# Kernel optimization log

Hardware: AMD Instinct MI355X
Metric: run time of the kernel (lower is better)

Reference implementation:

```python
import jax, jax.numpy as jnp
import numpy as np

C = 256
HEADS = 4
HIDDEN = 4 * C  # LeFF default hidden_dim = dim*4
EPS = 1e-5


def conv2d(x, w, pad):
    # x: [B,C,H,W], w: [O,I,kh,kw]
    return jax.lax.conv_general_dilated(
        x, w, window_strides=(1, 1), padding=[(pad, pad), (pad, pad)],
        dimension_numbers=('NCHW', 'OIHW', 'NCHW'))


def dwconv2d(x, w, pad):
    # depthwise: w: [C,1,kh,kw], groups = C
    return jax.lax.conv_general_dilated(
        x, w, window_strides=(1, 1), padding=[(pad, pad), (pad, pad)],
        dimension_numbers=('NCHW', 'OIHW', 'NCHW'),
        feature_group_count=x.shape[1])


def conv1x1(x, w):
    # w: [O, I]; pointwise conv as einsum
    return jnp.einsum('oi,bihw->bohw', w, x)


def layernorm(x, weight, bias):
    # WithBias LayerNorm over channel dim of NCHW (matches to_3d -> LN over c)
    mu = jnp.mean(x, axis=1, keepdims=True)
    var = jnp.mean((x - mu) ** 2, axis=1, keepdims=True)
    xn = (x - mu) / jnp.sqrt(var + EPS)
    return xn * weight[None, :, None, None] + bias[None, :, None, None]


def mhsa(q, k, v, heads):
    # q,k,v: [B,C,H,W] -> global attention over N = H*W tokens
    b, c, h, w = q.shape
    d = c // heads
    scale = d ** -0.5
    def split(t):
        return t.reshape(b, heads, d, h * w)  # [B,H,d,N]
    qh, kh, vh = split(q), split(k), split(v)
    attn = jnp.einsum('bhdn,bhdm->bhnm', qh, kh) * scale  # [B,H,N,N]
    attn = jax.nn.softmax(attn, axis=-1)
    out = jnp.einsum('bhnm,bhdm->bhdn', attn, vh)
    return out.reshape(b, c, h, w)


def self_attn(x, w_qkv, w_proj, heads):
    qkv = conv1x1(x, w_qkv)  # [B,3C,H,W]
    q, k, v = jnp.split(qkv, 3, axis=1)
    return conv1x1(mhsa(q, k, v, heads), w_proj)


def cross_attn(qf, kvf, w_q, w_k, w_v, w_proj, heads):
    q = conv1x1(qf, w_q)
    k = conv1x1(kvf, w_k)
    v = conv1x1(kvf, w_v)
    return conv1x1(mhsa(q, k, v, heads), w_proj)


def leff(x, w_in, w_dw, w_out):
    h = conv1x1(x, w_in)
    h = dwconv2d(h, w_dw, pad=1)
    h = jax.nn.gelu(h, approximate=False)  # torch nn.GELU() = exact erf
    return conv1x1(h, w_out)


def setup_inputs() -> dict:
    key = jax.random.key(0)
    ks = jax.random.split(key, 32)
    s = 0.02
    inp = {
        'aop_feat': jax.random.normal(ks[0], (8, C, 32, 32), jnp.float32),
        'dop_feat': jax.random.normal(ks[1], (8, C, 32, 32), jnp.float32),
        'w_qconv': jax.random.normal(ks[2], (C, C, 3, 3), jnp.float32) * s,
        'w_kvconv': jax.random.normal(ks[3], (C, C, 5, 5), jnp.float32) * s,
        'lnq1_w': jnp.ones((C,), jnp.float32), 'lnq1_b': jnp.zeros((C,), jnp.float32),
        'lnkv1_w': jnp.ones((C,), jnp.float32), 'lnkv1_b': jnp.zeros((C,), jnp.float32),
        'lnq2_w': jnp.ones((C,), jnp.float32), 'lnq2_b': jnp.zeros((C,), jnp.float32),
        'lnkv2_w': jnp.ones((C,), jnp.float32), 'lnkv2_b': jnp.zeros((C,), jnp.float32),
        'lnffn_w': jnp.ones((C,), jnp.float32), 'lnffn_b': jnp.zeros((C,), jnp.float32),
        'saq_qkv': jax.random.normal(ks[4], (3 * C, C), jnp.float32) * s,
        'saq_proj': jax.random.normal(ks[5], (C, C), jnp.float32) * s,
        'sakv_qkv': jax.random.normal(ks[6], (3 * C, C), jnp.float32) * s,
        'sakv_proj': jax.random.normal(ks[7], (C, C), jnp.float32) * s,
        'ca_q': jax.random.normal(ks[8], (C, C), jnp.float32) * s,
        'ca_k': jax.random.normal(ks[9], (C, C), jnp.float32) * s,
        'ca_v': jax.random.normal(ks[10], (C, C), jnp.float32) * s,
        'ca_proj': jax.random.normal(ks[11], (C, C), jnp.float32) * s,
        'leff_in': jax.random.normal(ks[12], (HIDDEN, C), jnp.float32) * s,
        'leff_dw': jax.random.normal(ks[13], (HIDDEN, 1, 3, 3), jnp.float32) * s,
        'leff_out': jax.random.normal(ks[14], (C, HIDDEN), jnp.float32) * s,
    }
    return inp


def reference(aop_feat, dop_feat, w_qconv, w_kvconv,
              lnq1_w, lnq1_b, lnkv1_w, lnkv1_b, lnq2_w, lnq2_b,
              lnkv2_w, lnkv2_b, lnffn_w, lnffn_b,
              saq_qkv, saq_proj, sakv_qkv, sakv_proj,
              ca_q, ca_k, ca_v, ca_proj,
              leff_in, leff_dw, leff_out):
    # q branch
    q_branch = conv2d(aop_feat, w_qconv, pad=1)
    q_branch = q_branch + self_attn(layernorm(q_branch, lnq1_w, lnq1_b), saq_qkv, saq_proj, HEADS)
    q = layernorm(q_branch, lnq2_w, lnq2_b)
    # kv branch
    kv_branch = conv2d(dop_feat, w_kvconv, pad=2)
    kv_branch = kv_branch + self_attn(layernorm(kv_branch, lnkv1_w, lnkv1_b), sakv_qkv, sakv_proj, HEADS)
    kv = layernorm(kv_branch, lnkv2_w, lnkv2_b)
    # cross attention + FFN
    x = q_branch + cross_attn(q, kv, ca_q, ca_k, ca_v, ca_proj, HEADS)
    x = x + leff(layernorm(x, lnffn_w, lnffn_b), leff_in, leff_dw, leff_out)
    return x
```

## Files before the change

### kernel.cpp

```cpp
#include <hip/hip_runtime.h>
#include <hip/hip_bf16.h>


using bf16 = __hip_bfloat16;
typedef short v8s __attribute__((ext_vector_type(8)));
typedef float v4f  __attribute__((ext_vector_type(4)));

static __device__ __forceinline__ float bf2f(bf16 x) { return __bfloat162float(x); }
static __device__ __forceinline__ float us2f(unsigned short u)
{ union { unsigned int i; float f; } x; x.i = ((unsigned)u) << 16; return x.f; }
static __device__ __forceinline__ unsigned short f2us(float f)
{ bf16 h = __float2bfloat16(f); return *(unsigned short*)&h; }
static __device__ __forceinline__ float ldi(const void* p, size_t i, int isbf)
{ return isbf ? bf2f(((const bf16*)p)[i]) : ((const float*)p)[i]; }

__global__ void detect_kernel(const unsigned short* p, int* flag)
{
    if (threadIdx.x == 0 && blockIdx.x == 0)
        *flag = (p[0] == 0x3F80) ? 1 : 0;
}

struct CvtArgs { const void* src[20]; unsigned off[21]; };

__global__ __launch_bounds__(256) void pre_all(
    CvtArgs a,
    const void* __restrict__ s0, const void* __restrict__ s1,
    const void* __restrict__ W3, const void* __restrict__ W5,
    const void* __restrict__ Wdw, const int* __restrict__ flag,
    bf16* __restrict__ canon,
    bf16* __restrict__ d0, bf16* __restrict__ d1,
    bf16* __restrict__ R3, bf16* __restrict__ R5, bf16* __restrict__ Rdw)
{
    __shared__ float T[64][65];
    int bx = blockIdx.x, t = threadIdx.x;
    int isbf = *flag;
    if (bx < 5130) {
        unsigned e = bx * 256u + t;
        int s = 0;
        while (e >= a.off[s + 1]) ++s;
        canon[e] = __float2bfloat16(ldi(a.src[s], e - a.off[s], isbf));
    } else if (bx < 6154) {
        int i = bx - 5130;
        int x = i & 15, y = (i >> 4) & 3, z = i >> 6;
        const void* src = (z < 8) ? s0 : s1;
        bf16* dst       = (z < 8) ? d0 : d1;
        int hw0 = x * 64, c0 = y * 64, b = z & 7;
        int c = t >> 2, x16 = (t & 3) * 16;
        size_t sbase = ((size_t)b * 256 + c0 + c) * 1024 + hw0 + x16;
#pragma unroll
        for (int j = 0; j < 16; ++j) T[c][x16 + j] = ldi(src, sbase + j, isbf);
        __syncthreads();
        int hw = t >> 2, c16 = (t & 3) * 16;
        bf16* dp = dst + ((size_t)(b << 10) + hw0 + hw) * 256 + c0 + c16;
#pragma unroll
        for (int j = 0; j < 16; ++j) dp[j] = __float2bfloat16(T[c16 + j][hw]);
    } else {
        int idx = (bx - 6154) * 256 + t;
        if (idx < 589824) {
            int ci = idx & 255, o = (idx >> 8) & 255, khkw = idx >> 16;
            int kh = khkw / 3, kw = khkw % 3;
            R3[idx] = __float2bfloat16(
                ldi(W3, (((size_t)o * 256 + ci) * 3 + kh) * 3 + kw, isbf));
        } else if (idx < 2228224) {
            int j = idx - 589824;
            int ci = j & 255, o = (j >> 8) & 255, khkw = j >> 16;
            int kh = khkw / 5, kw = khkw % 5;
            R5[j] = __float2bfloat16(
                ldi(W5, (((size_t)o * 256 + ci) * 5 + kh) * 5 + kw, isbf));
        } else {
            int j = idx - 2228224;
            int c = j & 1023, tap = j >> 10;
            Rdw[j] = __float2bfloat16(ldi(Wdw, (size_t)c * 9 + tap, isbf));
        }
    }
}

static __device__ __forceinline__ void gemm_store(
    bf16* __restrict__ Yb, float* __restrict__ Yf, bf16* __restrict__ Y2,
    const bf16* __restrict__ R, int mode, int Ochan,
    int mm, int nn, float v)
{
    if (mode == 0) {
        size_t off = (size_t)mm * Ochan + nn;
        if (R) v += bf2f(R[off]);
        Yb[off] = __float2bfloat16(v);
    } else if (mode == 1) {
        Yb[((size_t)(nn >> 10) * Ochan + mm) * 1024 + (nn & 1023)] =
            __float2bfloat16(v);
    } else if (mode == 2) {
        Yf[((size_t)(nn >> 10) * Ochan + mm) * 1024 + (nn & 1023)] =
            v + bf2f(R[(size_t)nn * 256 + mm]);
    } else if (mode == 3) {
        if (mm < 512) Yb[(size_t)nn * 512 + mm] = __float2bfloat16(v);
        else Y2[((size_t)(nn >> 10) * 256 + (mm - 512)) * 1024 + (nn & 1023)] =
                 __float2bfloat16(v);
    } else {
        Yb[(size_t)nn * 512 + Ochan + mm] = __float2bfloat16(v);
    }
}

static __device__ __forceinline__ void mgemm_core(
    const short* __restrict__ MA, const short* __restrict__ MB,
    bf16* __restrict__ Yb, float* __restrict__ Yf, bf16* __restrict__ Y2,
    const bf16* __restrict__ R, int K, int mode, int Ochan,
    short As[64][72], short Bs[64][72])
{
    int m0 = blockIdx.x * 64, n0 = blockIdx.y * 64;
    int t = threadIdx.x, lane = t & 63, wv = t >> 6;
    int l15 = lane & 15, quad = lane >> 4;
    int srow = t >> 2, scol = (t & 3) * 16;

    const short* pa = &MA[(size_t)(m0 + srow) * K + scol];
    const short* pb = &MB[(size_t)(n0 + srow) * K + scol];

    v4f acc[4] = {};
    v8s ra0 = *(const v8s*)&pa[0], ra1 = *(const v8s*)&pa[8];
    v8s rb0 = *(const v8s*)&pb[0], rb1 = *(const v8s*)&pb[8];

    for (int k0 = 0; k0 < K; k0 += 64) {
        if (k0) __syncthreads();
        *(v8s*)&As[srow][scol]     = ra0;
        *(v8s*)&As[srow][scol + 8] = ra1;
        *(v8s*)&Bs[srow][scol]     = rb0;
        *(v8s*)&Bs[srow][scol + 8] = rb1;
        __syncthreads();
        if (k0 + 64 < K) {
            ra0 = *(const v8s*)&pa[k0 + 64];
            ra1 = *(const v8s*)&pa[k0 + 72];
            rb0 = *(const v8s*)&pb[k0 + 64];
            rb1 = *(const v8s*)&pb[k0 + 72];
        }
#pragma unroll
        for (int kk = 0; kk < 2; ++kk) {
            v8s a = *(const v8s*)&As[wv * 16 + l15][kk * 32 + quad * 8];
#pragma unroll
            for (int nt = 0; nt < 4; ++nt) {
                v8s b = *(const v8s*)&Bs[nt * 16 + l15][kk * 32 + quad * 8];
                acc[nt] = __builtin_amdgcn_mfma_f32_16x16x32_bf16(a, b, acc[nt], 0, 0, 0);
            }
        }
    }

#pragma unroll
    for (int nt = 0; nt < 4; ++nt)
#pragma unroll
        for (int r = 0; r < 4; ++r)
            gemm_store(Yb, Yf, Y2, R, mode, Ochan,
                       m0 + wv * 16 + quad * 4 + r,
                       n0 + nt * 16 + l15, acc[nt][r]);
}

__global__ __launch_bounds__(256) void mgemm(
    const short* __restrict__ MA, const short* __restrict__ MB,
    bf16* __restrict__ Yb, float* __restrict__ Yf, bf16* __restrict__ Y2,
    const bf16* __restrict__ R, int K, int mode, int Ochan)
{
    __shared__ short As[64][72], Bs[64][72];
    mgemm_core(MA, MB, Yb, Yf, Y2, R, K, mode, Ochan, As, Bs);
}

struct GA { const short* A; const short* B; bf16* Yb; float* Yf; bf16* Y2;
            const bf16* R; int K; int mode; int Oc; };
struct GA3 { GA g[3]; };

__global__ __launch_bounds__(256) void mgemm_z(GA3 P)
{
    __shared__ short As[64][72], Bs[64][72];
    const GA& a = P.g[blockIdx.z];
    mgemm_core(a.A, a.B, a.Yb, a.Yf, a.Y2, a.R, a.K, a.mode, a.Oc, As, Bs);
}

template <int KS, int PAD>
static __device__ __forceinline__ void mconv128_core(
    const short* __restrict__ Xn, const short* __restrict__ Wr,
    bf16* __restrict__ Y, float* __restrict__ Yf,
    short As[128][72], short Bs[128][72],
    int p0, int o0, int kbeg, int kend)
{
    int t = threadIdx.x, lane = t & 63, wv = t >> 6;
    int l15 = lane & 15, quad = lane >> 4;
    int wm = wv >> 1, wn = wv & 1;
    int srow = t >> 1, scol = (t & 1) * 32;

    int p  = p0 + srow;
    int hw = p & 1023, hh = hw >> 5, ww = hw & 31;
    size_t ib = ((size_t)(p >> 10)) << 10;

    v4f acc[4][4] = {};
    v8s ra[4], rb[4];

    auto ldk = [&](int k0) {
        int khkw = k0 >> 8;
        int kh = khkw / KS, kw = khkw % KS;
        int hi = hh + kh - PAD, wi = ww + kw - PAD;
        int aci = (k0 & 255) + scol;
        v8s z = {0, 0, 0, 0, 0, 0, 0, 0};
        ra[0] = z; ra[1] = z; ra[2] = z; ra[3] = z;
        if ((unsigned)hi < 32u && (unsigned)wi < 32u) {
            const short* sa = &Xn[(ib + (hi << 5) + wi) * 256 + aci];
            ra[0] = *(const v8s*)&sa[0];  ra[1] = *(const v8s*)&sa[8];
            ra[2] = *(const v8s*)&sa[16]; ra[3] = *(const v8s*)&sa[24];
        }
        const short* sb = &Wr[((size_t)khkw * 256 + o0 + srow) * 256 + (k0 & 255) + scol];
        rb[0] = *(const v8s*)&sb[0];  rb[1] = *(const v8s*)&sb[8];
        rb[2] = *(const v8s*)&sb[16]; rb[3] = *(const v8s*)&sb[24];
    };

    ldk(kbeg);

    for (int k0 = kbeg; k0 < kend; k0 += 64) {
        if (k0 != kbeg) __syncthreads();
        *(v8s*)&As[srow][scol]      = ra[0];
        *(v8s*)&As[srow][scol + 8]  = ra[1];
        *(v8s*)&As[srow][scol + 16] = ra[2];
        *(v8s*)&As[srow][scol + 24] = ra[3];
        *(v8s*)&Bs[srow][scol]      = rb[0];
        *(v8s*)&Bs[srow][scol + 8]  = rb[1];
        *(v8s*)&Bs[srow][scol + 16] = rb[2];
        *(v8s*)&Bs[srow][scol + 24] = rb[3];
        __syncthreads();
        if (k0 + 64 < kend) ldk(k0 + 64);
#pragma unroll
        for (int kk = 0; kk < 2; ++kk) {
            v8s af[4], bf[4];
#pragma unroll
            for (int i = 0; i < 4; ++i)
                af[i] = *(const v8s*)&As[wm * 64 + i * 16 + l15][kk * 32 + quad * 8];
#pragma unroll
            for (int i = 0; i < 4; ++i)
                bf[i] = *(const v8s*)&Bs[wn * 64 + i * 16 + l15][kk * 32 + quad * 8];
#pragma unroll
            for (int mt = 0; mt < 4; ++mt)
#pragma unroll
                for (int nt = 0; nt < 4; ++nt)
                    acc[mt][nt] = __builtin_amdgcn_mfma_f32_16x16x32_bf16(
                        af[mt], bf[nt], acc[mt][nt], 0, 0, 0);
        }
    }

#pragma unroll
    for (int mt = 0; mt < 4; ++mt)
#pragma unroll
        for (int nt = 0; nt < 4; ++nt)
#pragma unroll
            for (int r = 0; r < 4; ++r) {
                int pp = p0 + wm * 64 + mt * 16 + quad * 4 + r;
                int oo = o0 + wn * 64 + nt * 16 + l15;
                if (Yf) Yf[(size_t)pp * 256 + oo] = acc[mt][nt][r];
                else    Y[(size_t)pp * 256 + oo] = __float2bfloat16(acc[mt][nt][r]);
            }
}

__global__ __launch_bounds__(256) void mconv2(
    const short* __restrict__ Xa, const short* __restrict__ Wa, bf16* __restrict__ Ya,
    const short* __restrict__ Xb, const short* __restrict__ Wb,
    float* __restrict__ P0, float* __restrict__ P1, float* __restrict__ P2)
{
    __shared__ short As[128][72];
    __shared__ short Bs[128][72];
    int wg = blockIdx.x;
    if (wg < 128) {
        mconv128_core<3, 1>(Xa, Wa, Ya, nullptr, As, Bs,
                            (wg & 63) * 128, (wg >> 6) * 128, 0, 2304);
    } else {
        int j = wg - 128;
        int part = j >> 7, xy = j & 127;
        float* Pf = (part == 0) ? P0 : (part == 1) ? P1 : P2;
        int kbeg = part * 2112;
        int kend = (part < 2) ? kbeg + 2112 : 6400;
        mconv128_core<5, 2>(Xb, Wb, nullptr, Pf, As, Bs,
                            (xy & 63) * 128, (xy >> 6) * 128, kbeg, kend);
    }
}

__global__ __launch_bounds__(256) void addcvt3(
    const float* __restrict__ A, const float* __restrict__ B,
    const float* __restrict__ C, bf16* __restrict__ Y)
{
    int i = (blockIdx.x * 256 + threadIdx.x) * 4;
    float4 a = *(const float4*)&A[i];
    float4 b = *(const float4*)&B[i];
    float4 c = *(const float4*)&C[i];
    ushort4 o;
    o.x = f2us(a.x + b.x + c.x);
    o.y = f2us(a.y + b.y + c.y);
    o.z = f2us(a.z + b.z + c.z);
    o.w = f2us(a.w + b.w + c.w);
    *(ushort4*)((unsigned short*)Y + i) = o;
}

static __device__ __forceinline__ void attn_core(
    const bf16* __restrict__ QK, const bf16* __restrict__ V,
    bf16* __restrict__ Out, int b, int h, int n0,
    short Ps[4][16][72], short Ks[64][72], short Vs[64][72])
{
    int t = threadIdx.x, lane = t & 63, wv = t >> 6;
    int l15 = lane & 15, quad = lane >> 4;
    int srow = t >> 2, scol = (t & 3) * 16;

    const short* qk = (const short*)QK;
    const short* vp = (const short*)V + ((size_t)b * 256 + h * 64) * 1024;

    size_t qrow = ((size_t)b * 1024 + n0 + wv * 16 + l15) * 512 + h * 64;
    v8s qf0 = *(const v8s*)&qk[qrow + quad * 8];
    v8s qf1 = *(const v8s*)&qk[qrow + 32 + quad * 8];

    v4f oacc[4] = {};
    float mi[4], li[4], nmiSC[4];
#pragma unroll
    for (int r = 0; r < 4; ++r) { mi[r] = -1e30f; li[r] = 0.f; nmiSC[r] = 0.f; }
    const float SC = 0.18033688011112042f;

    const short* kbase = &qk[((size_t)b * 1024 + srow) * 512 + 256 + h * 64 + scol];
    const short* vbase = vp + (size_t)srow * 1024 + scol;

    v8s rk0 = *(const v8s*)&kbase[0], rk1 = *(const v8s*)&kbase[8];
    v8s rv0 = *(const v8s*)&vbase[0], rv1 = *(const v8s*)&vbase[8];

    for (int m0 = 0; m0 < 1024; m0 += 64) {
        if (m0) __syncthreads();
        *(v8s*)&Ks[srow][scol]     = rk0;
        *(v8s*)&Ks[srow][scol + 8] = rk1;
        *(v8s*)&Vs[srow][scol]     = rv0;
        *(v8s*)&Vs[srow][scol + 8] = rv1;
        __syncthreads();
        if (m0 + 64 < 1024) {
            rk0 = *(const v8s*)&kbase[(size_t)(m0 + 64) * 512];
            rk1 = *(const v8s*)&kbase[(size_t)(m0 + 64) * 512 + 8];
            rv0 = *(const v8s*)&vbase[m0 + 64];
            rv1 = *(const v8s*)&vbase[m0 + 72];
        }

        v4f sacc[4];
        __builtin_amdgcn_s_setprio(1);
#pragma unroll
        for (int ct = 0; ct < 4; ++ct) {
            v8s kf0 = *(const v8s*)&Ks[ct * 16 + l15][quad * 8];
            v8s kf1 = *(const v8s*)&Ks[ct * 16 + l15][32 + quad * 8];
            v4f z = {0.f, 0.f, 0.f, 0.f};
            z = __builtin_amdgcn_mfma_f32_16x16x32_bf16(qf0, kf0, z, 0, 0, 0);
            z = __builtin_amdgcn_mfma_f32_16x16x32_bf16(qf1, kf1, z, 0, 0, 0);
            sacc[ct] = z;
        }
        __builtin_amdgcn_s_setprio(0);

        float pr[4];
#pragma unroll
        for (int r = 0; r < 4; ++r)
            pr[r] = fmaxf(fmaxf(sacc[0][r], sacc[1][r]),
                          fmaxf(sacc[2][r], sacc[3][r]));
        bool grow = (pr[0] > mi[0]) | (pr[1] > mi[1]) |
                    (pr[2] > mi[2]) | (pr[3] > mi[3]);
        if (__any(grow)) {
#pragma unroll
            for (int mk = 1; mk <= 8; mk <<= 1)
#pragma unroll
                for (int r = 0; r < 4; ++r)
                    pr[r] = fmaxf(pr[r], __shfl_xor(pr[r], mk));
#pragma unroll
            for (int r = 0; r < 4; ++r) {
                float mn = fmaxf(mi[r], pr[r]);
                float al = exp2f((mi[r] - mn) * SC);
                mi[r] = mn;
                nmiSC[r] = -mn * SC;
                li[r] *= al;
#pragma unroll
                for (int dt = 0; dt < 4; ++dt) oacc[dt][r] *= al;
            }
        }

#pragma unroll
        for (int ct = 0; ct < 4; ++ct)
#pragma unroll
            for (int r = 0; r < 4; ++r) {
                float pvv = exp2f(fmaf(sacc[ct][r], SC, nmiSC[r]));
                li[r] += pvv;
                Ps[wv][quad * 4 + r][ct * 16 + l15] = (short)f2us(pvv);
            }

        v8s pf0 = *(const v8s*)&Ps[wv][l15][quad * 8];
        v8s pf1 = *(const v8s*)&Ps[wv][l15][32 + quad * 8];
        __builtin_amdgcn_s_setprio(1);
#pragma unroll
        for (int dt = 0; dt < 4; ++dt) {
            v8s vf0 = *(const v8s*)&Vs[dt * 16 + l15][quad * 8];
            v8s vf1 = *(const v8s*)&Vs[dt * 16 + l15][32 + quad * 8];
            oacc[dt] = __builtin_amdgcn_mfma_f32_16x16x32_bf16(pf0, vf0, oacc[dt], 0, 0, 0);
            oacc[dt] = __builtin_amdgcn_mfma_f32_16x16x32_bf16(pf1, vf1, oacc[dt], 0, 0, 0);
        }
        __builtin_amdgcn_s_setprio(0);
    }

#pragma unroll
    for (int mk = 1; mk <= 8; mk <<= 1)
#pragma unroll
        for (int r = 0; r < 4; ++r)
            li[r] += __shfl_xor(li[r], mk);

    float linv[4];
#pragma unroll
    for (int r = 0; r < 4; ++r) linv[r] = 1.0f / li[r];
    size_t pb = (size_t)b * 1024 + n0 + wv * 16;
#pragma unroll
    for (int dt = 0; dt < 4; ++dt)
#pragma unroll
        for (int r = 0; r < 4; ++r)
            Out[(pb + quad * 4 + r) * 256 + h * 64 + dt * 16 + l15] =
                __float2bfloat16(oacc[dt][r] * linv[r]);
}

template <int NG>
__global__ __launch_bounds__(256) void attn_swz(
    const bf16* __restrict__ QK0, const bf16* __restrict__ V0, bf16* __restrict__ O0,
    const bf16* __restrict__ QK1, const bf16* __restrict__ V1, bf16* __restrict__ O1)
{
    __shared__ short Ps[4][16][72];
    __shared__ short Ks[64][72], Vs[64][72];
    int i = blockIdx.x;
    int xcd = i & 7, idx = i >> 3;
    int g = xcd * (NG / 8) + (idx >> 4);
    int n0 = (idx & 15) * 64;
    int h = g & 3, zz = g >> 2;
    int b = zz & 7;
    if (zz < 8) attn_core(QK0, V0, O0, b, h, n0, Ps, Ks, Vs);
    else        attn_core(QK1, V1, O1, b, h, n0, Ps, Ks, Vs);
}

static __device__ __forceinline__ void ln_row(
    const bf16* __restrict__ X, const bf16* __restrict__ g,
    const bf16* __restrict__ be, bf16* __restrict__ Y, size_t p)
{
    int lane = threadIdx.x & 63;
    const ushort4 u = *(const ushort4*)(X + p * 256 + lane * 4);
    float v0 = us2f(u.x), v1 = us2f(u.y), v2 = us2f(u.z), v3 = us2f(u.w);
    float s = v0 + v1 + v2 + v3;
    float ss = v0 * v0 + v1 * v1 + v2 * v2 + v3 * v3;
#pragma unroll
    for (int off = 32; off; off >>= 1) {
        s  += __shfl_xor(s, off);
        ss += __shfl_xor(ss, off);
    }
    float mu   = s * (1.0f / 256.0f);
    float var  = ss * (1.0f / 256.0f) - mu * mu;
    float rstd = rsqrtf(fmaxf(var, 0.0f) + 1e-5f);
    const ushort4 gu = *(const ushort4*)((const unsigned short*)g + lane * 4);
    const ushort4 bu = *(const ushort4*)((const unsigned short*)be + lane * 4);
    ushort4 o;
    o.x = f2us((v0 - mu) * rstd * us2f(gu.x) + us2f(bu.x));
    o.y = f2us((v1 - mu) * rstd * us2f(gu.y) + us2f(bu.y));
    o.z = f2us((v2 - mu) * rstd * us2f(gu.z) + us2f(bu.z));
    o.w = f2us((v3 - mu) * rstd * us2f(gu.w) + us2f(bu.w));
    *(ushort4*)(Y + p * 256 + lane * 4) = o;
}

__global__ __launch_bounds__(256) void ln_nhwc(
    const bf16* __restrict__ X, const bf16* __restrict__ g,
    const bf16* __restrict__ be, bf16* __restrict__ Y)
{
    int wv = threadIdx.x >> 6;
    ln_row(X, g, be, Y, (size_t)blockIdx.x * 4 + wv);
}

__global__ __launch_bounds__(256) void ln_nhwc2(
    const bf16* __restrict__ X0, const bf16* __restrict__ g0,
    const bf16* __restrict__ b0, bf16* __restrict__ Y0,
    const bf16* __restrict__ X1, const bf16* __restrict__ g1,
    const bf16* __restrict__ b1, bf16* __restrict__ Y1)
{
    int wv = threadIdx.x >> 6;
    int sel = blockIdx.x >> 11;
    size_t p = (size_t)(blockIdx.x & 2047) * 4 + wv;
    if (sel == 0) ln_row(X0, g0, b0, Y0, p);
    else          ln_row(X1, g1, b1, Y1, p);
}

__global__ __launch_bounds__(256) void dwgelu_nhwc(
    const bf16* __restrict__ H, const bf16* __restrict__ Wr,
    bf16* __restrict__ Y)
{
    int idx = blockIdx.x * 256 + threadIdx.x;
    int p = idx >> 7, c8 = (idx & 127) * 8;
    int hw = p & 1023, hh = hw >> 5, ww = hw & 31;
    size_t ib = ((size_t)(p >> 10)) << 10;
    float acc[8] = {};
#pragma unroll
    for (int kh = 0; kh < 3; ++kh)
#pragma unroll
        for (int kw = 0; kw < 3; ++kw) {
            int hi = hh + kh - 1, wi = ww + kw - 1;
            if ((unsigned)hi < 32u && (unsigned)wi < 32u) {
                v8s hv = *(const v8s*)((const short*)H + (ib + (hi << 5) + wi) * 1024 + c8);
                v8s wvv = *(const v8s*)((const short*)Wr + (kh * 3 + kw) * 1024 + c8);
#pragma unroll
                for (int j = 0; j < 8; ++j)
                    acc[j] = fmaf(us2f((unsigned short)wvv[j]),
                                  us2f((unsigned short)hv[j]), acc[j]);
            }
        }
    short ov[8];
#pragma unroll
    for (int j = 0; j < 8; ++j) {
        float x = acc[j];
        ov[j] = (short)f2us(0.5f * x * (1.0f + erff(x * 0.70710678118654752f)));
    }
    v8s o = {ov[0], ov[1], ov[2], ov[3], ov[4], ov[5], ov[6], ov[7]};
    *(v8s*)((short*)Y + (size_t)p * 1024 + c8) = o;
}

extern "C" void kernel_launch(void* const* d_in, const int* in_sizes, int n_in,
                              void* d_out, int out_size, void* d_ws, size_t ws_size,
                              hipStream_t stream)
{
    static const int  lidx[20] = {4,5,6,7,8,9,10,11,12,13,14,15,16,17,18,19,20,21,22,24};
    static const unsigned lsz[20] = {256,256,256,256,256,256,256,256,256,256,
                                     196608,65536,196608,65536,
                                     65536,65536,65536,65536,262144,262144};
    CvtArgs args;
    unsigned pre[21]; pre[0] = 0;
    for (int i = 0; i < 20; ++i) {
        args.src[i] = d_in[lidx[i]];
        pre[i + 1] = pre[i] + lsz[i];
    }
    for (int i = 0; i < 21; ++i) args.off[i] = pre[i];
    const unsigned ltot = pre[20];

    int*  flag  = (int*)d_ws;
    bf16* canon = (bf16*)d_ws + 128;
    bf16* cn[25];
    for (int i = 0; i < 20; ++i) cn[lidx[i]] = canon + pre[i];

    bf16* Wr3  = canon + ltot;
    bf16* Wr5  = Wr3 + 589824;
    bf16* Wdwr = Wr5 + 1638400;
    const size_t SZ = 2097152;
    bf16* slab = Wdwr + 9216;
    bf16* qb   = slab + 0 * SZ;
    bf16* kvb  = slab + 1 * SZ;
    bf16* t0   = slab + 2 * SZ;
    bf16* q    = slab + 3 * SZ;
    bf16* kv   = slab + 4 * SZ;
    bf16* QKb  = slab + 5 * SZ;
    bf16* Vb   = slab + 7 * SZ;
    bf16* t1   = slab + 8 * SZ;
    bf16* QK2  = slab + 9 * SZ;
    bf16* V2   = slab + 11 * SZ;
    bf16* aopT = slab + 9 * SZ;
    bf16* dopT = slab + 10 * SZ;
    bf16* hb   = slab + 3 * SZ;
    bf16* h2   = slab + 7 * SZ;
    float* P0f = (float*)(slab + 2 * SZ);
    float* P1f = (float*)(slab + 4 * SZ);
    float* P2f = (float*)(slab + 6 * SZ);
    float* out = (float*)d_out;

    dim3 blk(256);
    auto S = [](const bf16* p) { return (const short*)p; };

    detect_kernel<<<1, 64, 0, stream>>>((const unsigned short*)d_in[4], flag);
    pre_all<<<5130 + 1024 + 8740, blk, 0, stream>>>(
        args, d_in[0], d_in[1], d_in[2], d_in[3], d_in[23], flag,
        canon, aopT, dopT, Wr3, Wr5, Wdwr);

    mconv2<<<512, blk, 0, stream>>>(S(aopT), (const short*)Wr3, qb,
                                    S(dopT), (const short*)Wr5, P0f, P1f, P2f);
    addcvt3<<<2048, blk, 0, stream>>>(P0f, P1f, P2f, kvb);

    ln_nhwc2<<<4096, blk, 0, stream>>>(qb, cn[4], cn[5], t0,
                                       kvb, cn[6], cn[7], t1);
    GA3 P;
    P.g[0] = GA{S(cn[14]), S(t0), QKb, nullptr, Vb, nullptr, 256, 3, 0};
    P.g[1] = GA{S(cn[16]), S(t1), QK2, nullptr, V2, nullptr, 256, 3, 0};
    P.g[2] = P.g[1];
    mgemm_z<<<dim3(12, 128, 2), blk, 0, stream>>>(P);

    attn_swz<64><<<1024, blk, 0, stream>>>(QKb, Vb, t0, QK2, V2, t1);

    P.g[0] = GA{S(t0), S(cn[15]), qb, nullptr, nullptr, qb, 256, 0, 256};
    P.g[1] = GA{S(t1), S(cn[17]), kvb, nullptr, nullptr, kvb, 256, 0, 256};
    P.g[2] = P.g[1];
    mgemm_z<<<dim3(128, 4, 2), blk, 0, stream>>>(P);

    ln_nhwc2<<<4096, blk, 0, stream>>>(qb, cn[8], cn[9], q,
                                       kvb, cn[10], cn[11], kv);

    P.g[0] = GA{S(cn[18]), S(q),  QKb, nullptr, nullptr, nullptr, 256, 4, 0};
    P.g[1] = GA{S(cn[19]), S(kv), QKb, nullptr, nullptr, nullptr, 256, 4, 256};
    P.g[2] = GA{S(cn[20]), S(kv), Vb,  nullptr, nullptr, nullptr, 256, 1, 256};
    mgemm_z<<<dim3(4, 128, 3), blk, 0, stream>>>(P);

    attn_swz<32><<<512, blk, 0, stream>>>(QKb, Vb, t0, QKb, Vb, t0);
    mgemm<<<dim3(128, 4), blk, 0, stream>>>(S(t0), S(cn[21]), qb, nullptr, nullptr, qb, 256, 0, 256);

    ln_nhwc<<<2048, blk, 0, stream>>>(qb, cn[12], cn[13], t0);
    mgemm<<<dim3(128, 16), blk, 0, stream>>>(S(t0), S(cn[22]), hb, nullptr, nullptr, nullptr, 256, 0, 1024);
    dwgelu_nhwc<<<4096, blk, 0, stream>>>(hb, Wdwr, h2);
    mgemm<<<dim3(4, 128), blk, 0, stream>>>(S(cn[24]), S(h2), nullptr, out, nullptr, qb, 1024, 2, 256);
}
```

Baseline: 402.2 us.

## Keep attention probabilities in registers via transposed MFMA and permuted K rows

The QK^T and PV MFMAs now have their operands swapped, so each lane holds scores for a single query row. K rows are read with a permutation chosen so that the exp'd probabilities can be packed directly into the B operand of the PV MFMA. This removes the Ps shared-memory round trip and cuts the row-max and row-sum shuffles from four per row to two. Output stores become vectorized 4-element writes. The cost is subtle index bookkeeping that must be exactly right for correctness.

```diff
diff --git a/kernel.cpp b/kernel.cpp
--- a/kernel.cpp
+++ b/kernel.cpp
@@ -292,7 +292,7 @@
 static __device__ __forceinline__ void attn_core(
     const bf16* __restrict__ QK, const bf16* __restrict__ V,
     bf16* __restrict__ Out, int b, int h, int n0,
-    short Ps[4][16][72], short Ks[64][72], short Vs[64][72])
+    short Ks[64][72], short Vs[64][72])
 {
     int t = threadIdx.x, lane = t & 63, wv = t >> 6;
     int l15 = lane & 15, quad = lane >> 4;
@@ -306,10 +306,13 @@
     v8s qf1 = *(const v8s*)&qk[qrow + 32 + quad * 8];
 
     v4f oacc[4] = {};
-    float mi[4], li[4], nmiSC[4];
-#pragma unroll
-    for (int r = 0; r < 4; ++r) { mi[r] = -1e30f; li[r] = 0.f; nmiSC[r] = 0.f; }
+    float mi = -1e30f, li = 0.f, nmi = 0.f;
     const float SC = 0.18033688011112042f;
+
+    int sig[4];
+#pragma unroll
+    for (int ct = 0; ct < 4; ++ct)
+        sig[ct] = ((ct & 1) << 5) + ((l15 >> 2) << 3) + ((ct >> 1) << 2) + (l15 & 3);
 
     const short* kbase = &qk[((size_t)b * 1024 + srow) * 512 + 256 + h * 64 + scol];
     const short* vbase = vp + (size_t)srow * 1024 + scol;
@@ -335,78 +338,74 @@
         __builtin_amdgcn_s_setprio(1);
 #pragma unroll
         for (int ct = 0; ct < 4; ++ct) {
-            v8s kf0 = *(const v8s*)&Ks[ct * 16 + l15][quad * 8];
-            v8s kf1 = *(const v8s*)&Ks[ct * 16 + l15][32 + quad * 8];
+            v8s kf0 = *(const v8s*)&Ks[sig[ct]][quad * 8];
+            v8s kf1 = *(const v8s*)&Ks[sig[ct]][32 + quad * 8];
             v4f z = {0.f, 0.f, 0.f, 0.f};
-            z = __builtin_amdgcn_mfma_f32_16x16x32_bf16(qf0, kf0, z, 0, 0, 0);
-            z = __builtin_amdgcn_mfma_f32_16x16x32_bf16(qf1, kf1, z, 0, 0, 0);
+            z = __builtin_amdgcn_mfma_f32_16x16x32_bf16(kf0, qf0, z, 0, 0, 0);
+            z = __builtin_amdgcn_mfma_f32_16x16x32_bf16(kf1, qf1, z, 0, 0, 0);
             sacc[ct] = z;
         }
         __builtin_amdgcn_s_setprio(0);
 
-        float pr[4];
-#pragma unroll
-        for (int r = 0; r < 4; ++r)
-            pr[r] = fmaxf(fmaxf(sacc[0][r], sacc[1][r]),
-                          fmaxf(sacc[2][r], sacc[3][r]));
-        bool grow = (pr[0] > mi[0]) | (pr[1] > mi[1]) |
-                    (pr[2] > mi[2]) | (pr[3] > mi[3]);
-        if (__any(grow)) {
-#pragma unroll
-            for (int mk = 1; mk <= 8; mk <<= 1)
-#pragma unroll
-                for (int r = 0; r < 4; ++r)
-                    pr[r] = fmaxf(pr[r], __shfl_xor(pr[r], mk));
+        float pm = sacc[0][0];
+#pragma unroll
+        for (int ct = 0; ct < 4; ++ct)
+#pragma unroll
+            for (int r = 0; r < 4; ++r) pm = fmaxf(pm, sacc[ct][r]);
+        if (__any(pm > mi)) {
+            pm = fmaxf(pm, __shfl_xor(pm, 16));
+            pm = fmaxf(pm, __shfl_xor(pm, 32));
+            float mn = fmaxf(mi, pm);
+            float al = exp2f((mi - mn) * SC);
+            mi = mn;
+            nmi = -mn * SC;
+            li *= al;
+#pragma unroll
+            for (int dt = 0; dt < 4; ++dt)
+#pragma unroll
+                for (int r = 0; r < 4; ++r) oacc[dt][r] *= al;
+        }
+
+        short pv[4][4];
+#pragma unroll
+        for (int ct = 0; ct < 4; ++ct)
 #pragma unroll
             for (int r = 0; r < 4; ++r) {
-                float mn = fmaxf(mi[r], pr[r]);
-                float al = exp2f((mi[r] - mn) * SC);
-                mi[r] = mn;
-                nmiSC[r] = -mn * SC;
-                li[r] *= al;
-#pragma unroll
-                for (int dt = 0; dt < 4; ++dt) oacc[dt][r] *= al;
+                float pvv = exp2f(fmaf(sacc[ct][r], SC, nmi));
+                li += pvv;
+                pv[ct][r] = (short)f2us(pvv);
             }
-        }
-
-#pragma unroll
-        for (int ct = 0; ct < 4; ++ct)
-#pragma unroll
-            for (int r = 0; r < 4; ++r) {
-                float pvv = exp2f(fmaf(sacc[ct][r], SC, nmiSC[r]));
-                li[r] += pvv;
-                Ps[wv][quad * 4 + r][ct * 16 + l15] = (short)f2us(pvv);
-            }
-
-        v8s pf0 = *(const v8s*)&Ps[wv][l15][quad * 8];
-        v8s pf1 = *(const v8s*)&Ps[wv][l15][32 + quad * 8];
+
+        v8s pf0 = {pv[0][0], pv[0][1], pv[0][2], pv[0][3],
+                   pv[2][0], pv[2][1], pv[2][2], pv[2][3]};
+        v8s pf1 = {pv[1][0], pv[1][1], pv[1][2], pv[1][3],
+                   pv[3][0], pv[3][1], pv[3][2], pv[3][3]};
+
         __builtin_amdgcn_s_setprio(1);
 #pragma unroll
         for (int dt = 0; dt < 4; ++dt) {
             v8s vf0 = *(const v8s*)&Vs[dt * 16 + l15][quad * 8];
             v8s vf1 = *(const v8s*)&Vs[dt * 16 + l15][32 + quad * 8];
-            oacc[dt] = __builtin_amdgcn_mfma_f32_16x16x32_bf16(pf0, vf0, oacc[dt], 0, 0, 0);
-            oacc[dt] = __builtin_amdgcn_mfma_f32_16x16x32_bf16(pf1, vf1, oacc[dt], 0, 0, 0);
+            oacc[dt] = __builtin_amdgcn_mfma_f32_16x16x32_bf16(vf0, pf0, oacc[dt], 0, 0, 0);
+            oacc[dt] = __builtin_amdgcn_mfma_f32_16x16x32_bf16(vf1, pf1, oacc[dt], 0, 0, 0);
         }
         __builtin_amdgcn_s_setprio(0);
     }
 
-#pragma unroll
-    for (int mk = 1; mk <= 8; mk <<= 1)
-#pragma unroll
-        for (int r = 0; r < 4; ++r)
-            li[r] += __shfl_xor(li[r], mk);
-
-    float linv[4];
-#pragma unroll
-    for (int r = 0; r < 4; ++r) linv[r] = 1.0f / li[r];
-    size_t pb = (size_t)b * 1024 + n0 + wv * 16;
-#pragma unroll
-    for (int dt = 0; dt < 4; ++dt)
-#pragma unroll
-        for (int r = 0; r < 4; ++r)
-            Out[(pb + quad * 4 + r) * 256 + h * 64 + dt * 16 + l15] =
-                __float2bfloat16(oacc[dt][r] * linv[r]);
+    li += __shfl_xor(li, 16);
+    li += __shfl_xor(li, 32);
+    float linv = 1.0f / li;
+
+    size_t orow = ((size_t)b * 1024 + n0 + wv * 16 + l15) * 256 + h * 64;
+#pragma unroll
+    for (int dt = 0; dt < 4; ++dt) {
+        ushort4 o;
+        o.x = f2us(oacc[dt][0] * linv);
+        o.y = f2us(oacc[dt][1] * linv);
+        o.z = f2us(oacc[dt][2] * linv);
+        o.w = f2us(oacc[dt][3] * linv);
+        *(ushort4*)((unsigned short*)Out + orow + dt * 16 + quad * 4) = o;
+    }
 }
 
 template <int NG>
@@ -414,7 +413,6 @@
     const bf16* __restrict__ QK0, const bf16* __restrict__ V0, bf16* __restrict__ O0,
     const bf16* __restrict__ QK1, const bf16* __restrict__ V1, bf16* __restrict__ O1)
 {
-    __shared__ short Ps[4][16][72];
     __shared__ short Ks[64][72], Vs[64][72];
     int i = blockIdx.x;
     int xcd = i & 7, idx = i >> 3;
@@ -422,8 +420,8 @@
     int n0 = (idx & 15) * 64;
     int h = g & 3, zz = g >> 2;
     int b = zz & 7;
-    if (zz < 8) attn_core(QK0, V0, O0, b, h, n0, Ps, Ks, Vs);
-    else        attn_core(QK1, V1, O1, b, h, n0, Ps, Ks, Vs);
+    if (zz < 8) attn_core(QK0, V0, O0, b, h, n0, Ks, Vs);
+    else        attn_core(QK1, V1, O1, b, h, n0, Ks, Vs);
 }
 
 static __device__ __forceinline__ void ln_row(
```

New measurement: 382.7 us. 1.05x faster.
